# Kernel tuning notes

Hardware: AMD Instinct MI355X
Metric: run time of the kernel (lower is better)

## Reference

```python
import jax, jax.numpy as jnp
import numpy as np
from jax import lax

T, K, F = 262144, 20, 16


def setup_inputs() -> dict:
    key = jax.random.key(0)
    k1, k2, k3, k4 = jax.random.split(key, 4)
    return {
        "observations": jax.random.normal(k1, (T, F), dtype=jnp.float32),
        "beta_logits": jax.random.normal(k2, (K,), dtype=jnp.float32),
        "pi_logits": jax.random.normal(k3, (K, K), dtype=jnp.float32),
        "means": jax.random.normal(k4, (K, F), dtype=jnp.float32),
        "log_vars": jnp.zeros((K, F), dtype=jnp.float32),
    }


def _stick_breaking(logits):
    b = jax.nn.sigmoid(logits)
    cp = jnp.cumprod(1.0 - b)
    return b * jnp.concatenate([jnp.ones((1,), logits.dtype), cp[:-1]])


def _emission_logp(obs, means, log_vars):
    # Diagonal-covariance MultivariateNormal log_prob, vectorized over T and K
    # without materializing a [T,K,F] intermediate.
    var = jnp.exp(log_vars) + 1e-6                       # [K,F]
    inv = 1.0 / var
    const = jnp.sum(means * means * inv + jnp.log(2.0 * jnp.pi * var), axis=1)  # [K]
    quad = (obs * obs) @ inv.T - 2.0 * (obs @ (means * inv).T)                  # [T,K]
    return -0.5 * (quad + const[None, :])


def reference(observations, beta_logits, pi_logits, means, log_vars):
    w = _stick_breaking(beta_logits)                      # [K]
    P = jax.nn.softmax(pi_logits, axis=1)                 # [K,K]
    em = _emission_logp(observations, means, log_vars)    # [T,K]

    # Forward recursion (normalized alpha, as in the original)
    a0 = w * jnp.exp(em[0])
    a0 = a0 / (a0.sum() + 1e-10)

    def fstep(a, e):
        x = (a @ P) * jnp.exp(e)
        x = x / (x.sum() + 1e-10)
        return x, x

    _, a_rest = lax.scan(fstep, a0, em[1:])
    alpha = jnp.concatenate([a0[None], a_rest], axis=0)   # [T,K]

    # Backward recursion (normalized beta)
    bT = jnp.ones((K,), observations.dtype)

    def bstep(bn, e):
        x = P @ (bn * jnp.exp(e))
        x = x / (x.sum() + 1e-10)
        return x, x

    _, b_rest = lax.scan(bstep, bT, em[1:], reverse=True)
    beta = jnp.concatenate([b_rest, bT[None]], axis=0)    # [T,K]

    log_likelihood = jnp.log(alpha[-1].sum() + 1e-10)
    return alpha, beta, log_likelihood
```

## Files before the change

kernel.cpp:

```cpp
#include <hip/hip_runtime.h>
#include <hip/hip_fp16.h>


namespace {
constexpr int Tn = 262144;
constexpr int Kn = 20;
constexpr int Fn = 16;
constexpr float EPSF = 1e-10f;
constexpr float TINY = 1e-35f;

constexpr int Ln3 = 16;
constexpr int Wn3 = 20;
constexpr int NC3 = Tn / Ln3;
constexpr int NBF = NC3 / 16;
constexpr int NBS3 = NC3 / 4;
constexpr int SPC = Ln3 * Kn;

constexpr size_t OFF_P    = 0;
constexpr size_t OFF_W    = 400;
constexpr size_t OFF_CK   = 420;
constexpr size_t OFF_MVIV = 440;
constexpr size_t OFF_E    = 1152;
constexpr size_t OFF_MF   = OFF_E + (size_t)Tn*20 + 64;
constexpr size_t OFF_MB   = OFF_MF + (size_t)Tn;
constexpr size_t OFF_MATF = OFF_MB + (size_t)Tn;
constexpr size_t OFF_MATB = OFF_MATF + 4*(size_t)NC3;
constexpr size_t OFF_SF   = OFF_MATB + 4*(size_t)NC3;
constexpr size_t OFF_SB   = OFF_SF + NC3;
constexpr size_t OFF_END  = OFF_SB + NC3;
}

#if __has_builtin(__builtin_amdgcn_rcpf)
#define FRCP(x) __builtin_amdgcn_rcpf(x)
#else
#define FRCP(x) (1.0f/(x))
#endif

template<int CTRL>
__device__ __forceinline__ float dpp_add(float v) {
  int s = __builtin_amdgcn_update_dpp(0, __float_as_int(v), CTRL, 0xF, 0xF, true);
  return v + __int_as_float(s);
}

__device__ __forceinline__ float reduce16(float v) {
  v = dpp_add<0xB1>(v);
  v = dpp_add<0x4E>(v);
  v = dpp_add<0x141>(v);
  v = dpp_add<0x140>(v);
  return v;
}

__global__ __launch_bounds__(64) void prep_kernel(
    const float* beta_logits, const float* pi_logits,
    const float* means, const float* log_vars, float* ws)
{
  int k = threadIdx.x;
  if (k < Kn) {
    float row[Kn];
    float mx = -1e30f;
#pragma unroll
    for (int j = 0; j < Kn; ++j) { row[j] = pi_logits[k*Kn + j]; mx = fmaxf(mx, row[j]); }
    float s = 0.f;
#pragma unroll
    for (int j = 0; j < Kn; ++j) { row[j] = expf(row[j] - mx); s += row[j]; }
    float invs = 1.0f / s;
#pragma unroll
    for (int j = 0; j < Kn; ++j) ws[OFF_P + k*Kn + j] = row[j] * invs;
    float ck = 0.f;
#pragma unroll
    for (int f = 0; f < Fn; ++f) {
      float lv  = log_vars[k*Fn + f];
      float var = expf(lv) + 1e-6f;
      float iv  = 1.0f / var;
      float mu  = means[k*Fn + f];
      ((float2*)(ws + OFF_MVIV))[k*Fn + f] = make_float2(mu * iv, iv);
      ck += mu*mu*iv + logf(6.2831853071795864f * var);
    }
    ws[OFF_CK + k] = ck;
  } else if (k == Kn) {
    float cp = 1.f;
#pragma unroll
    for (int i = 0; i < Kn; ++i) {
      float b = 1.0f / (1.0f + expf(-beta_logits[i]));
      ws[OFF_W + i] = b * cp;
      cp *= (1.0f - b);
    }
  }
}

__global__ __launch_bounds__(320) void emis_kernel(const float* __restrict__ obs, float* ws)
{
  __shared__ __align__(16) float so[64][20];
  __shared__ __align__(16) float scm[16][24];
  __shared__ __align__(16) float scv[16][24];
  __shared__ __align__(16) float sck[20];
  const int tid = threadIdx.x;
  const int t0 = blockIdx.x * 64;

  if (tid < 256) {
    float4 v = ((const float4*)(obs + (size_t)t0 * Fn))[tid];
    int r = tid >> 2, j = tid & 3;
    *(float4*)&so[r][j*4] = v;
  } else {
    int i = tid - 256;
#pragma unroll
    for (int q = 0; q < 5; ++q) {
      int idx = i * 5 + q;
      float2 c2 = ((const float2*)(ws + OFF_MVIV))[idx];
      int k = idx >> 4, f = idx & 15;
      scm[f][k] = c2.x;
      scv[f][k] = c2.y;
    }
    if (i < Kn) sck[i] = ws[OFF_CK + i];
  }
  __syncthreads();

  const int tl = tid / 5;
  const int k0 = (tid - tl*5) * 4;

  float o[16];
  *(float4*)&o[0]  = *(const float4*)&so[tl][0];
  *(float4*)&o[4]  = *(const float4*)&so[tl][4];
  *(float4*)&o[8]  = *(const float4*)&so[tl][8];
  *(float4*)&o[12] = *(const float4*)&so[tl][12];

  float s1x=0.f,s1y=0.f,s1z=0.f,s1w=0.f;
  float s2x=0.f,s2y=0.f,s2z=0.f,s2w=0.f;
#pragma unroll
  for (int f = 0; f < Fn; ++f) {
    float4 cm = *(const float4*)&scm[f][k0];
    float4 cv = *(const float4*)&scv[f][k0];
    float ov = o[f];
    s1x = fmaf(cv.x * ov, ov, s1x); s2x = fmaf(cm.x, ov, s2x);
    s1y = fmaf(cv.y * ov, ov, s1y); s2y = fmaf(cm.y, ov, s2y);
    s1z = fmaf(cv.z * ov, ov, s1z); s2z = fmaf(cm.z, ov, s2z);
    s1w = fmaf(cv.w * ov, ov, s1w); s2w = fmaf(cm.w, ov, s2w);
  }
  float4 ckv = *(const float4*)&sck[k0];
  float4 rr;
  rr.x = __expf(fmaf(-0.5f, s1x + ckv.x, s2x));
  rr.y = __expf(fmaf(-0.5f, s1y + ckv.y, s2y));
  rr.z = __expf(fmaf(-0.5f, s1z + ckv.z, s2z));
  rr.w = __expf(fmaf(-0.5f, s1w + ckv.w, s2w));
  *(float4*)(ws + OFF_E + (size_t)(t0 + tl)*20 + k0) = rr;
}

__global__ __launch_bounds__(256) void scan3_kernel(float* ws, float* out)
{
  __shared__ __align__(16) float xsh[16][20];
  const int tid = threadIdx.x;
  const int g   = tid >> 4;
  const int ll  = tid & 15;
  const bool hi = (ll < 4);
  const int l4  = 16 + (ll & 3);
  const bool isF = ((int)blockIdx.x < NBF);
  const int c = (isF ? (int)blockIdx.x : (int)blockIdx.x - NBF) * 16 + g;
  const float* E = ws + OFF_E;
  float* xg = &xsh[g][0];

  float Pv0[Kn], Pv1[Kn];
#pragma unroll
  for (int k = 0; k < Kn; ++k) {
    if (isF) {
      Pv0[k] = ws[OFF_P + k*Kn + ll];
      float p1 = ws[OFF_P + k*Kn + l4];
      Pv1[k] = hi ? p1 : 0.f;
    } else {
      Pv0[k] = ws[OFF_P + ll*Kn + k];
      float p1 = ws[OFF_P + l4*Kn + k];
      Pv1[k] = hi ? p1 : 0.f;
    }
  }

  float Ma = 1.f, Mc = 0.f, Md = 1.f;
  float* mArr = ws + (isF ? OFF_MF : OFF_MB);
  __half* uH = (__half*)(out + (isF ? (size_t)0 : (size_t)Tn * Kn) + (size_t)c * SPC);

  auto mobius = [&](float m) {
    float na = m * Ma;
    float nc = fmaf(EPSF, Mc, na);
    float nd = EPSF * Md;
    float mx = fmaxf(nc, nd);
    float lam = (mx > 0.f) ? FRCP(mx) : 1.0f;
    Ma = na*lam; Mc = nc*lam; Md = nd*lam;
  };
  auto matvec2 = [&](float& r0, float& r1) {
    float xv[20];
    *(float4*)&xv[0]  = *(const float4*)&xg[0];
    *(float4*)&xv[4]  = *(const float4*)&xg[4];
    *(float4*)&xv[8]  = *(const float4*)&xg[8];
    *(float4*)&xv[12] = *(const float4*)&xg[12];
    *(float4*)&xv[16] = *(const float4*)&xg[16];
    float A0 = xv[0]*Pv0[0], A1 = xv[1]*Pv0[1];
    float B0 = xv[0]*Pv1[0], B1 = xv[1]*Pv1[1];
#pragma unroll
    for (int k = 2; k < 20; k += 2) {
      A0 = fmaf(xv[k],   Pv0[k],   A0);
      A1 = fmaf(xv[k+1], Pv0[k+1], A1);
      B0 = fmaf(xv[k],   Pv1[k],   B0);
      B1 = fmaf(xv[k+1], Pv1[k+1], B1);
    }
    r0 = A0 + A1; r1 = B0 + B1;
  };

  if (isF) {
    const int bodyStart = c * Ln3;
    const int tend = bodyStart + Ln3 - 1;
    const int t0 = (c == 0) ? 0 : (bodyStart - Wn3);
    float e0a = E[t0*20 + ll],     e1a = E[t0*20 + l4];
    float v0, v1;
    if (c == 0) {
      v0 = ws[OFF_W + ll] * e0a;
      v1 = hi ? ws[OFF_W + l4] * e1a : 0.f;
    } else {
      v0 = 0.05f * e0a;
      v1 = hi ? 0.05f * e1a : 0.f;
    }
    float sv = reduce16(v0 + v1);
    float m = sv;
    float iV = (sv > TINY) ? FRCP(sv) : 1.0f;
    if (sv <= TINY) { v0 = 0.05f; v1 = hi ? 0.05f : 0.f; }
    if (c == 0) {
      if (ll == 0) mArr[0] = m;
      mobius(m);
      uH[ll] = __float2half(v0 * iV);
      if (hi) uH[l4] = __float2half(v1 * iV);
    }
    float A = m * iV;
    float rho = (m > TINY) ? FRCP(m) : 1.0f;
    float e0b = E[(t0+1)*20 + ll], e1b = E[(t0+1)*20 + l4];
    float e0c = E[(t0+2)*20 + ll], e1c = E[(t0+2)*20 + l4];

#define FWD_STEP(REC)                                                     \
    {                                                                     \
      xg[ll] = v0;                                                        \
      if (hi) xg[16 + ll] = v1;                                           \
      float acc0, acc1; matvec2(acc0, acc1);                              \
      float er0 = e0a * rho, er1 = e1a * rho;                             \
      e0a = e0b; e0b = e0c; e0c = E[(t+3)*20 + ll];                       \
      e1a = e1b; e1b = e1c; e1c = E[(t+3)*20 + l4];                       \
      v0 = acc0 * er0; v1 = acc1 * er1;                                   \
      float sv2 = reduce16(v0 + v1);                                      \
      float mn = sv2 * A;                                                 \
      float iVn = (sv2 > TINY) ? FRCP(sv2) : 1.0f;                        \
      if (sv2 <= TINY) { v0 = 0.05f; v1 = hi ? 0.05f : 0.f; }             \
      if (REC) {                                                          \
        if (ll == 0) mArr[t] = mn;                                        \
        mobius(mn);                                                       \
        int lt = t - bodyStart;                                           \
        uH[lt*Kn + ll] = __float2half(v0 * iVn);                          \
        if (hi) uH[lt*Kn + 16 + ll] = __float2half(v1 * iVn);             \
      }                                                                   \
      A = mn * iVn;                                                       \
      rho = (mn > TINY) ? FRCP(mn) : 1.0f;                                \
    }

    for (int t = t0 + 1; t < bodyStart; ++t) FWD_STEP(false)
    const int bstart2 = (c == 0) ? 1 : bodyStart;
    for (int t = bstart2; t <= tend; ++t) FWD_STEP(true)
#undef FWD_STEP
    if (ll == 0) ((float4*)(ws + OFF_MATF))[c] = make_float4(Ma, Mc, Md, 0.f);
  } else {
    const int bodyStart = c * Ln3;
    const int top = bodyStart + Ln3 - 1;
    int r0 = top + Wn3; if (r0 > Tn - 1) r0 = Tn - 1;
    float v0 = 0.05f, v1 = hi ? 0.05f : 0.f;
    float sv = reduce16(v0 + v1);
    float iV = (sv > TINY) ? FRCP(sv) : 1.0f;
    float A = iV;
    float rho = 1.0f;
    float e0a = E[r0*20 + ll],     e1a = E[r0*20 + l4];
    float e0b = E[(r0-1)*20 + ll], e1b = E[(r0-1)*20 + l4];
    float e0c = E[(r0-2)*20 + ll], e1c = E[(r0-2)*20 + l4];

#define BWD_STEP(REC)                                                     \
    {                                                                     \
      xg[ll] = v0 * e0a;                                                  \
      if (hi) xg[16 + ll] = v1 * e1a;                                     \
      float acc0, acc1; matvec2(acc0, acc1);                              \
      v0 = acc0 * rho; v1 = acc1 * rho;                                   \
      e0a = e0b; e0b = e0c; e0c = E[(r-2)*20 + ll];                       \
      e1a = e1b; e1b = e1c; e1c = E[(r-2)*20 + l4];                       \
      float sv2 = reduce16(v0 + v1);                                      \
      float mn = sv2 * A;                                                 \
      float iVn = (sv2 > TINY) ? FRCP(sv2) : 1.0f;                        \
      if (sv2 <= TINY) { v0 = 0.05f; v1 = hi ? 0.05f : 0.f; }             \
      if (REC) {                                                          \
        if (ll == 0) mArr[r+1] = mn;                                      \
        mobius(mn);                                                       \
        int lr = r - bodyStart;                                           \
        uH[lr*Kn + ll] = __float2half(v0 * iVn);                          \
        if (hi) uH[lr*Kn + 16 + ll] = __float2half(v1 * iVn);             \
      }                                                                   \
      A = mn * iVn;                                                       \
      rho = (mn > TINY) ? FRCP(mn) : 1.0f;                                \
    }

    for (int r = r0 - 1; r > top; --r) BWD_STEP(false)
    int rb = (r0 - 1 < top) ? (r0 - 1) : top;
    for (int r = rb; r >= bodyStart; --r) BWD_STEP(true)
#undef BWD_STEP
    if (ll == 0) ((float4*)(ws + OFF_MATB))[NC3 - 1 - c] = make_float4(Ma, Mc, Md, 0.f);
  }
}

__global__ __launch_bounds__(1024) void combine4_kernel(float* ws, float* out)
{
  __shared__ float wag[16][3];
  __shared__ float wpre[16][3];
  const bool isF = (blockIdx.x == 0);
  const float4* M4 = (const float4*)(ws + (isF ? OFF_MATF : OFF_MATB));
  float* sArr = ws + (isF ? OFF_SF : OFF_SB);
  const float s0 = isF ? 1.0f : 20.0f;
  constexpr int PG = NC3 / 1024;
  const int tid  = threadIdx.x;
  const int lane = tid & 63;
  const int wid  = tid >> 6;

  float4 mm[PG];
#pragma unroll
  for (int i = 0; i < PG; ++i) mm[i] = M4[tid*PG + i];

  float a = 1.f, cc = 0.f, d = 1.f;
#pragma unroll
  for (int i = 0; i < PG; ++i) {
    float na = mm[i].x * a;
    float nc = fmaf(mm[i].y, a, mm[i].z * cc);
    float nd = mm[i].z * d;
    float mx = fmaxf(na, fmaxf(nc, nd));
    float lam = (mx > 0.f) ? FRCP(mx) : 1.0f;
    a = na*lam; cc = nc*lam; d = nd*lam;
  }

  float ia = a, ic = cc, id = d;
  for (int off = 1; off < 64; off <<= 1) {
    float pa = __shfl_up(ia, off, 64);
    float pc = __shfl_up(ic, off, 64);
    float pd = __shfl_up(id, off, 64);
    if (lane >= off) {
      float na = ia * pa;
      float nc = fmaf(ic, pa, id * pc);
      float nd = id * pd;
      float mx = fmaxf(na, fmaxf(nc, nd));
      float lam = (mx > 0.f) ? FRCP(mx) : 1.0f;
      ia = na*lam; ic = nc*lam; id = nd*lam;
    }
  }
  if (lane == 63) { wag[wid][0] = ia; wag[wid][1] = ic; wag[wid][2] = id; }
  __syncthreads();

  if (tid == 0) {
    float ea = 1.f, ec = 0.f, ed = 1.f;
#pragma unroll
    for (int w = 0; w < 16; ++w) {
      wpre[w][0] = ea; wpre[w][1] = ec; wpre[w][2] = ed;
      float na = wag[w][0] * ea;
      float nc = fmaf(wag[w][1], ea, wag[w][2] * ec);
      float nd = wag[w][2] * ed;
      float mx = fmaxf(na, fmaxf(nc, nd));
      float lam = (mx > 0.f) ? FRCP(mx) : 1.0f;
      ea = na*lam; ec = nc*lam; ed = nd*lam;
    }
    if (isF) {
      float den = fmaf(ec, s0, ed);
      float sfin = (den > 0.f) ? (ea * s0)/den : 0.f;
      out[(size_t)2 * Tn * Kn] = logf(sfin + EPSF);
    }
  }
  __syncthreads();

  float ea = __shfl_up(ia, 1, 64);
  float ec = __shfl_up(ic, 1, 64);
  float ed = __shfl_up(id, 1, 64);
  if (lane == 0) { ea = 1.f; ec = 0.f; ed = 1.f; }
  float pa = wpre[wid][0], pc = wpre[wid][1], pd = wpre[wid][2];
  float xa = ea * pa;
  float xc = fmaf(ec, pa, ed * pc);
  float xd = ed * pd;

  float num = xa * s0, den = fmaf(xc, s0, xd);
  float s = (den > 0.f) ? num/den : 0.f;
#pragma unroll
  for (int i = 0; i < PG; ++i) {
    sArr[tid*PG + i] = s;
    float nn = mm[i].x * s, dd = fmaf(mm[i].y, s, mm[i].z);
    s = (dd > 0.f) ? nn/dd : 0.f;
  }
}

__global__ __launch_bounds__(128) void scale3_kernel(float* ws, float* out)
{
  __shared__ float sig[4][Ln3];
  const int tid = threadIdx.x;
  const int g   = tid >> 5;
  const int jj  = tid & 31;
  const bool isF = ((int)blockIdx.x < NBS3);
  const int c = (isF ? (int)blockIdx.x : (int)blockIdx.x - NBS3) * 4 + g;
  float* base = out + (isF ? (size_t)0 : (size_t)Tn * Kn) + (size_t)c * SPC;
  const __half* hp = (const __half*)base;

  if (isF) {
    const float* mArr = ws + OFF_MF;
    float s = ws[OFF_SF + c];
    const int t0 = c * Ln3;
#pragma unroll
    for (int i = 0; i < Ln3; ++i) {
      float mm = mArr[t0 + i];
      float z = s * mm;
      float sn = z * FRCP(z + EPSF);
      if (jj == 0) sig[g][i] = sn;
      s = sn;
    }
  } else {
    const float* mArr = ws + OFF_MB;
    const int slot = NC3 - 1 - c;
    float s = ws[OFF_SB + slot];
    const int bodyStart = c * Ln3;
    const int top = bodyStart + Ln3 - 1;
#pragma unroll
    for (int r = top; r >= bodyStart; --r) {
      if (r == Tn - 1) {
        if (jj == 0) sig[g][Ln3 - 1] = 1.0f;
        continue;
      }
      float mm = mArr[r + 1];
      float z = s * mm;
      float sn = z * FRCP(z + EPSF);
      if (jj == 0) sig[g][r - bodyStart] = sn;
      s = sn;
    }
  }

  float vals[10];
#pragma unroll
  for (int q = 0; q < 10; ++q) vals[q] = __half2float(hp[jj*10 + q]);
  __syncthreads();

  const int tl = jj >> 1;
  float sg = sig[g][tl];
  const bool onesRow = (!isF && c == NC3 - 1 && tl == Ln3 - 1);
#pragma unroll
  for (int q = 0; q < 10; ++q) {
    float vv = onesRow ? 1.0f : vals[q] * sg;
    base[jj*10 + q] = vv;
  }
}

extern "C" void kernel_launch(void* const* d_in, const int* in_sizes, int n_in,
                              void* d_out, int out_size, void* d_ws, size_t ws_size,
                              hipStream_t stream) {
  const float* obs         = (const float*)d_in[0];
  const float* beta_logits = (const float*)d_in[1];
  const float* pi_logits   = (const float*)d_in[2];
  const float* means       = (const float*)d_in[3];
  const float* log_vars    = (const float*)d_in[4];
  float* out = (float*)d_out;
  float* ws  = (float*)d_ws;

  hipLaunchKernelGGL(prep_kernel, dim3(1), dim3(64), 0, stream,
                     beta_logits, pi_logits, means, log_vars, ws);
  hipLaunchKernelGGL(emis_kernel, dim3(Tn/64), dim3(320), 0, stream, obs, ws);
  hipLaunchKernelGGL(scan3_kernel, dim3(2*NBF), dim3(256), 0, stream, ws, out);
  hipLaunchKernelGGL(combine4_kernel, dim3(2), dim3(1024), 0, stream, ws, out);
  hipLaunchKernelGGL(scale3_kernel, dim3(2*NBS3), dim3(128), 0, stream, ws, out);
}
```

Measured before the change: 107.8 us.

## Split each scan chunk across 8 lanes with 3 states each, pack half2 outputs

```diff
diff --git a/kernel.cpp b/kernel.cpp
--- a/kernel.cpp
+++ b/kernel.cpp
@@ -10,10 +10,10 @@
 constexpr float TINY = 1e-35f;
 
 constexpr int Ln3 = 16;
-constexpr int Wn3 = 20;
+constexpr int Wn3 = 16;
 constexpr int NC3 = Tn / Ln3;
-constexpr int NBF = NC3 / 16;
-constexpr int NBS3 = NC3 / 4;
+constexpr int NBF4 = NC3 / 32;
+constexpr int NBSC = NC3 / 8;
 constexpr int SPC = Ln3 * Kn;
 
 constexpr size_t OFF_P    = 0;
@@ -42,12 +42,16 @@
   return v + __int_as_float(s);
 }
 
-__device__ __forceinline__ float reduce16(float v) {
+__device__ __forceinline__ float reduce8(float v) {
   v = dpp_add<0xB1>(v);
   v = dpp_add<0x4E>(v);
   v = dpp_add<0x141>(v);
-  v = dpp_add<0x140>(v);
   return v;
+}
+
+__device__ __forceinline__ unsigned packh2(float a, float b) {
+  __half2 h2 = __floats2half2_rn(a, b);
+  return *(unsigned*)&h2;
 }
 
 __global__ __launch_bounds__(64) void prep_kernel(
@@ -145,36 +149,37 @@
   *(float4*)(ws + OFF_E + (size_t)(t0 + tl)*20 + k0) = rr;
 }
 
-__global__ __launch_bounds__(256) void scan3_kernel(float* ws, float* out)
+__global__ __launch_bounds__(256, 4) void scan4_kernel(float* ws, float* out)
 {
-  __shared__ __align__(16) float xsh[16][20];
+  __shared__ __align__(16) float xsh[32][20];
   const int tid = threadIdx.x;
-  const int g   = tid >> 4;
-  const int ll  = tid & 15;
-  const bool hi = (ll < 4);
-  const int l4  = 16 + (ll & 3);
-  const bool isF = ((int)blockIdx.x < NBF);
-  const int c = (isF ? (int)blockIdx.x : (int)blockIdx.x - NBF) * 16 + g;
+  const int g   = tid >> 3;
+  const int j   = tid & 7;
+  const int q   = j & 3;
+  const int s1i = 8 + j;
+  const int s2i = 16 + q;
+  const bool isF = ((int)blockIdx.x < NBF4);
+  const int c = (isF ? (int)blockIdx.x : (int)blockIdx.x - NBF4) * 32 + g;
   const float* E = ws + OFF_E;
   float* xg = &xsh[g][0];
 
-  float Pv0[Kn], Pv1[Kn];
+  float Pv0[Kn], Pv1[Kn], Pv2[Kn];
 #pragma unroll
   for (int k = 0; k < Kn; ++k) {
     if (isF) {
-      Pv0[k] = ws[OFF_P + k*Kn + ll];
-      float p1 = ws[OFF_P + k*Kn + l4];
-      Pv1[k] = hi ? p1 : 0.f;
+      Pv0[k] = ws[OFF_P + k*Kn + j];
+      Pv1[k] = ws[OFF_P + k*Kn + s1i];
+      Pv2[k] = ws[OFF_P + k*Kn + s2i];
     } else {
-      Pv0[k] = ws[OFF_P + ll*Kn + k];
-      float p1 = ws[OFF_P + l4*Kn + k];
-      Pv1[k] = hi ? p1 : 0.f;
+      Pv0[k] = ws[OFF_P + j*Kn + k];
+      Pv1[k] = ws[OFF_P + s1i*Kn + k];
+      Pv2[k] = ws[OFF_P + s2i*Kn + k];
     }
   }
 
   float Ma = 1.f, Mc = 0.f, Md = 1.f;
   float* mArr = ws + (isF ? OFF_MF : OFF_MB);
-  __half* uH = (__half*)(out + (isF ? (size_t)0 : (size_t)Tn * Kn) + (size_t)c * SPC);
+  unsigned* uS = (unsigned*)(out + (isF ? (size_t)0 : (size_t)Tn * Kn) + (size_t)c * SPC);
 
   auto mobius = [&](float m) {
     float na = m * Ma;
@@ -184,72 +189,75 @@
     float lam = (mx > 0.f) ? FRCP(mx) : 1.0f;
     Ma = na*lam; Mc = nc*lam; Md = nd*lam;
   };
-  auto matvec2 = [&](float& r0, float& r1) {
+  auto matvec3 = [&](float& r0, float& r1, float& r2) {
     float xv[20];
     *(float4*)&xv[0]  = *(const float4*)&xg[0];
     *(float4*)&xv[4]  = *(const float4*)&xg[4];
     *(float4*)&xv[8]  = *(const float4*)&xg[8];
     *(float4*)&xv[12] = *(const float4*)&xg[12];
     *(float4*)&xv[16] = *(const float4*)&xg[16];
-    float A0 = xv[0]*Pv0[0], A1 = xv[1]*Pv0[1];
-    float B0 = xv[0]*Pv1[0], B1 = xv[1]*Pv1[1];
+    float a0 = xv[0]*Pv0[0], a1 = xv[1]*Pv0[1];
+    float b0 = xv[0]*Pv1[0], b1 = xv[1]*Pv1[1];
+    float c0 = xv[0]*Pv2[0], c1 = xv[1]*Pv2[1];
 #pragma unroll
     for (int k = 2; k < 20; k += 2) {
-      A0 = fmaf(xv[k],   Pv0[k],   A0);
-      A1 = fmaf(xv[k+1], Pv0[k+1], A1);
-      B0 = fmaf(xv[k],   Pv1[k],   B0);
-      B1 = fmaf(xv[k+1], Pv1[k+1], B1);
-    }
-    r0 = A0 + A1; r1 = B0 + B1;
+      a0 = fmaf(xv[k],   Pv0[k],   a0);
+      a1 = fmaf(xv[k+1], Pv0[k+1], a1);
+      b0 = fmaf(xv[k],   Pv1[k],   b0);
+      b1 = fmaf(xv[k+1], Pv1[k+1], b1);
+      c0 = fmaf(xv[k],   Pv2[k],   c0);
+      c1 = fmaf(xv[k+1], Pv2[k+1], c1);
+    }
+    r0 = a0 + a1; r1 = b0 + b1; r2 = c0 + c1;
   };
 
   if (isF) {
     const int bodyStart = c * Ln3;
     const int tend = bodyStart + Ln3 - 1;
     const int t0 = (c == 0) ? 0 : (bodyStart - Wn3);
-    float e0a = E[t0*20 + ll],     e1a = E[t0*20 + l4];
-    float v0, v1;
+    float e0a = E[t0*20 + j], e1a = E[t0*20 + s1i], e2a = E[t0*20 + s2i];
+    float v0, v1, v2;
     if (c == 0) {
-      v0 = ws[OFF_W + ll] * e0a;
-      v1 = hi ? ws[OFF_W + l4] * e1a : 0.f;
+      v0 = ws[OFF_W + j]   * e0a;
+      v1 = ws[OFF_W + s1i] * e1a;
+      v2 = ws[OFF_W + s2i] * e2a;
     } else {
-      v0 = 0.05f * e0a;
-      v1 = hi ? 0.05f * e1a : 0.f;
-    }
-    float sv = reduce16(v0 + v1);
+      v0 = 0.05f * e0a; v1 = 0.05f * e1a; v2 = 0.05f * e2a;
+    }
+    float sv = reduce8(fmaf(0.5f, v2, v0 + v1));
     float m = sv;
     float iV = (sv > TINY) ? FRCP(sv) : 1.0f;
-    if (sv <= TINY) { v0 = 0.05f; v1 = hi ? 0.05f : 0.f; }
+    if (sv <= TINY) { v0 = 0.05f; v1 = 0.05f; v2 = 0.05f; }
     if (c == 0) {
-      if (ll == 0) mArr[0] = m;
+      mArr[0] = m;
       mobius(m);
-      uH[ll] = __float2half(v0 * iV);
-      if (hi) uH[l4] = __float2half(v1 * iV);
+      uS[j] = packh2(v0 * iV, v1 * iV);
+      uS[8 + q] = packh2(v2 * iV, 0.f);
     }
     float A = m * iV;
     float rho = (m > TINY) ? FRCP(m) : 1.0f;
-    float e0b = E[(t0+1)*20 + ll], e1b = E[(t0+1)*20 + l4];
-    float e0c = E[(t0+2)*20 + ll], e1c = E[(t0+2)*20 + l4];
+    float e0b = E[(t0+1)*20 + j], e1b = E[(t0+1)*20 + s1i], e2b = E[(t0+1)*20 + s2i];
+    float e0c = E[(t0+2)*20 + j], e1c = E[(t0+2)*20 + s1i], e2c = E[(t0+2)*20 + s2i];
 
 #define FWD_STEP(REC)                                                     \
     {                                                                     \
-      xg[ll] = v0;                                                        \
-      if (hi) xg[16 + ll] = v1;                                           \
-      float acc0, acc1; matvec2(acc0, acc1);                              \
-      float er0 = e0a * rho, er1 = e1a * rho;                             \
-      e0a = e0b; e0b = e0c; e0c = E[(t+3)*20 + ll];                       \
-      e1a = e1b; e1b = e1c; e1c = E[(t+3)*20 + l4];                       \
-      v0 = acc0 * er0; v1 = acc1 * er1;                                   \
-      float sv2 = reduce16(v0 + v1);                                      \
+      xg[j] = v0; xg[s1i] = v1; xg[s2i] = v2;                             \
+      float acc0, acc1, acc2; matvec3(acc0, acc1, acc2);                  \
+      float er0 = e0a * rho, er1 = e1a * rho, er2 = e2a * rho;            \
+      e0a = e0b; e0b = e0c; e0c = E[(t+3)*20 + j];                        \
+      e1a = e1b; e1b = e1c; e1c = E[(t+3)*20 + s1i];                      \
+      e2a = e2b; e2b = e2c; e2c = E[(t+3)*20 + s2i];                      \
+      v0 = acc0 * er0; v1 = acc1 * er1; v2 = acc2 * er2;                  \
+      float sv2 = reduce8(fmaf(0.5f, v2, v0 + v1));                      \
       float mn = sv2 * A;                                                 \
       float iVn = (sv2 > TINY) ? FRCP(sv2) : 1.0f;                        \
-      if (sv2 <= TINY) { v0 = 0.05f; v1 = hi ? 0.05f : 0.f; }             \
+      if (sv2 <= TINY) { v0 = 0.05f; v1 = 0.05f; v2 = 0.05f; }            \
       if (REC) {                                                          \
-        if (ll == 0) mArr[t] = mn;                                        \
+        mArr[t] = mn;                                                     \
         mobius(mn);                                                       \
         int lt = t - bodyStart;                                           \
-        uH[lt*Kn + ll] = __float2half(v0 * iVn);                          \
-        if (hi) uH[lt*Kn + 16 + ll] = __float2half(v1 * iVn);             \
+        uS[lt*12 + j] = packh2(v0 * iVn, v1 * iVn);                       \
+        uS[lt*12 + 8 + q] = packh2(v2 * iVn, 0.f);                        \
       }                                                                   \
       A = mn * iVn;                                                       \
       rho = (mn > TINY) ? FRCP(mn) : 1.0f;                                \
@@ -259,38 +267,38 @@
     const int bstart2 = (c == 0) ? 1 : bodyStart;
     for (int t = bstart2; t <= tend; ++t) FWD_STEP(true)
 #undef FWD_STEP
-    if (ll == 0) ((float4*)(ws + OFF_MATF))[c] = make_float4(Ma, Mc, Md, 0.f);
+    ((float4*)(ws + OFF_MATF))[c] = make_float4(Ma, Mc, Md, 0.f);
   } else {
     const int bodyStart = c * Ln3;
     const int top = bodyStart + Ln3 - 1;
     int r0 = top + Wn3; if (r0 > Tn - 1) r0 = Tn - 1;
-    float v0 = 0.05f, v1 = hi ? 0.05f : 0.f;
-    float sv = reduce16(v0 + v1);
+    float v0 = 0.05f, v1 = 0.05f, v2 = 0.05f;
+    float sv = reduce8(fmaf(0.5f, v2, v0 + v1));
     float iV = (sv > TINY) ? FRCP(sv) : 1.0f;
     float A = iV;
     float rho = 1.0f;
-    float e0a = E[r0*20 + ll],     e1a = E[r0*20 + l4];
-    float e0b = E[(r0-1)*20 + ll], e1b = E[(r0-1)*20 + l4];
-    float e0c = E[(r0-2)*20 + ll], e1c = E[(r0-2)*20 + l4];
+    float e0a = E[r0*20 + j], e1a = E[r0*20 + s1i], e2a = E[r0*20 + s2i];
+    float e0b = E[(r0-1)*20 + j], e1b = E[(r0-1)*20 + s1i], e2b = E[(r0-1)*20 + s2i];
+    float e0c = E[(r0-2)*20 + j], e1c = E[(r0-2)*20 + s1i], e2c = E[(r0-2)*20 + s2i];
 
 #define BWD_STEP(REC)                                                     \
     {                                                                     \
-      xg[ll] = v0 * e0a;                                                  \
-      if (hi) xg[16 + ll] = v1 * e1a;                                     \
-      float acc0, acc1; matvec2(acc0, acc1);                              \
-      v0 = acc0 * rho; v1 = acc1 * rho;                                   \
-      e0a = e0b; e0b = e0c; e0c = E[(r-2)*20 + ll];                       \
-      e1a = e1b; e1b = e1c; e1c = E[(r-2)*20 + l4];                       \
-      float sv2 = reduce16(v0 + v1);                                      \
+      xg[j] = v0 * e0a; xg[s1i] = v1 * e1a; xg[s2i] = v2 * e2a;           \
+      float acc0, acc1, acc2; matvec3(acc0, acc1, acc2);                  \
+      v0 = acc0 * rho; v1 = acc1 * rho; v2 = acc2 * rho;                  \
+      e0a = e0b; e0b = e0c; e0c = E[(r-2)*20 + j];                        \
+      e1a = e1b; e1b = e1c; e1c = E[(r-2)*20 + s1i];                      \
+      e2a = e2b; e2b = e2c; e2c = E[(r-2)*20 + s2i];                      \
+      float sv2 = reduce8(fmaf(0.5f, v2, v0 + v1));                      \
       float mn = sv2 * A;                                                 \
       float iVn = (sv2 > TINY) ? FRCP(sv2) : 1.0f;                        \
-      if (sv2 <= TINY) { v0 = 0.05f; v1 = hi ? 0.05f : 0.f; }             \
+      if (sv2 <= TINY) { v0 = 0.05f; v1 = 0.05f; v2 = 0.05f; }            \
       if (REC) {                                                          \
-        if (ll == 0) mArr[r+1] = mn;                                      \
+        mArr[r+1] = mn;                                                   \
         mobius(mn);                                                       \
         int lr = r - bodyStart;                                           \
-        uH[lr*Kn + ll] = __float2half(v0 * iVn);                          \
-        if (hi) uH[lr*Kn + 16 + ll] = __float2half(v1 * iVn);             \
+        uS[lr*12 + j] = packh2(v0 * iVn, v1 * iVn);                       \
+        uS[lr*12 + 8 + q] = packh2(v2 * iVn, 0.f);                        \
       }                                                                   \
       A = mn * iVn;                                                       \
       rho = (mn > TINY) ? FRCP(mn) : 1.0f;                                \
@@ -300,7 +308,7 @@
     int rb = (r0 - 1 < top) ? (r0 - 1) : top;
     for (int r = rb; r >= bodyStart; --r) BWD_STEP(true)
 #undef BWD_STEP
-    if (ll == 0) ((float4*)(ws + OFF_MATB))[NC3 - 1 - c] = make_float4(Ma, Mc, Md, 0.f);
+    ((float4*)(ws + OFF_MATB))[NC3 - 1 - c] = make_float4(Ma, Mc, Md, 0.f);
   }
 }
 
@@ -388,62 +396,78 @@
   }
 }
 
-__global__ __launch_bounds__(128) void scale3_kernel(float* ws, float* out)
+__global__ __launch_bounds__(128) void scale4_kernel(float* ws, float* out)
 {
-  __shared__ float sig[4][Ln3];
   const int tid = threadIdx.x;
-  const int g   = tid >> 5;
-  const int jj  = tid & 31;
-  const bool isF = ((int)blockIdx.x < NBS3);
-  const int c = (isF ? (int)blockIdx.x : (int)blockIdx.x - NBS3) * 4 + g;
+  const int g   = tid >> 4;
+  const int ll  = tid & 15;
+  const bool isF = ((int)blockIdx.x < NBSC);
+  const int c = (isF ? (int)blockIdx.x : (int)blockIdx.x - NBSC) * 8 + g;
   float* base = out + (isF ? (size_t)0 : (size_t)Tn * Kn) + (size_t)c * SPC;
-  const __half* hp = (const __half*)base;
-
+  const unsigned* uS = (const unsigned*)base;
+
+  float mySig = 1.0f;
   if (isF) {
-    const float* mArr = ws + OFF_MF;
+    const float* mA = ws + OFF_MF;
     float s = ws[OFF_SF + c];
     const int t0 = c * Ln3;
 #pragma unroll
     for (int i = 0; i < Ln3; ++i) {
-      float mm = mArr[t0 + i];
-      float z = s * mm;
+      float z = s * mA[t0 + i];
       float sn = z * FRCP(z + EPSF);
-      if (jj == 0) sig[g][i] = sn;
+      if (i == ll) mySig = sn;
       s = sn;
     }
   } else {
-    const float* mArr = ws + OFF_MB;
-    const int slot = NC3 - 1 - c;
-    float s = ws[OFF_SB + slot];
-    const int bodyStart = c * Ln3;
-    const int top = bodyStart + Ln3 - 1;
-#pragma unroll
-    for (int r = top; r >= bodyStart; --r) {
-      if (r == Tn - 1) {
-        if (jj == 0) sig[g][Ln3 - 1] = 1.0f;
-        continue;
+    const float* mA = ws + OFF_MB;
+    float s = ws[OFF_SB + (NC3 - 1 - c)];
+    const int top = c * Ln3 + Ln3 - 1;
+#pragma unroll
+    for (int i = 0; i < Ln3; ++i) {
+      int r = top - i;
+      float sn;
+      if (r == Tn - 1) sn = s;
+      else {
+        float z = s * mA[r + 1];
+        sn = z * FRCP(z + EPSF);
       }
-      float mm = mArr[r + 1];
-      float z = s * mm;
-      float sn = z * FRCP(z + EPSF);
-      if (jj == 0) sig[g][r - bodyStart] = sn;
+      if (i == Ln3 - 1 - ll) mySig = sn;
       s = sn;
     }
   }
 
-  float vals[10];
-#pragma unroll
-  for (int q = 0; q < 10; ++q) vals[q] = __half2float(hp[jj*10 + q]);
+  uint4 ua = ((const uint4*)(uS + ll*12))[0];
+  uint4 ub = ((const uint4*)(uS + ll*12))[1];
+  uint4 uc = ((const uint4*)(uS + ll*12))[2];
   __syncthreads();
 
-  const int tl = jj >> 1;
-  float sg = sig[g][tl];
-  const bool onesRow = (!isF && c == NC3 - 1 && tl == Ln3 - 1);
-#pragma unroll
-  for (int q = 0; q < 10; ++q) {
-    float vv = onesRow ? 1.0f : vals[q] * sg;
-    base[jj*10 + q] = vv;
-  }
+  const bool onesRow = (!isF && c == NC3 - 1 && ll == Ln3 - 1);
+  float sg = mySig;
+  unsigned slots[12] = {ua.x,ua.y,ua.z,ua.w, ub.x,ub.y,ub.z,ub.w, uc.x,uc.y,uc.z,uc.w};
+  float o[20];
+#pragma unroll
+  for (int jj = 0; jj < 8; ++jj) {
+    __half2 h2 = *(__half2*)&slots[jj];
+    float2 f2 = __half22float2(h2);
+    o[jj]     = f2.x * sg;
+    o[8 + jj] = f2.y * sg;
+  }
+#pragma unroll
+  for (int qq = 0; qq < 4; ++qq) {
+    __half2 h2 = *(__half2*)&slots[8 + qq];
+    float2 f2 = __half22float2(h2);
+    o[16 + qq] = f2.x * sg;
+  }
+  if (onesRow) {
+#pragma unroll
+    for (int k = 0; k < 20; ++k) o[k] = 1.0f;
+  }
+  float* dst = base + ll * 20;
+  *(float4*)&dst[0]  = *(float4*)&o[0];
+  *(float4*)&dst[4]  = *(float4*)&o[4];
+  *(float4*)&dst[8]  = *(float4*)&o[8];
+  *(float4*)&dst[12] = *(float4*)&o[12];
+  *(float4*)&dst[16] = *(float4*)&o[16];
 }
 
 extern "C" void kernel_launch(void* const* d_in, const int* in_sizes, int n_in,
@@ -460,7 +484,7 @@
   hipLaunchKernelGGL(prep_kernel, dim3(1), dim3(64), 0, stream,
                      beta_logits, pi_logits, means, log_vars, ws);
   hipLaunchKernelGGL(emis_kernel, dim3(Tn/64), dim3(320), 0, stream, obs, ws);
-  hipLaunchKernelGGL(scan3_kernel, dim3(2*NBF), dim3(256), 0, stream, ws, out);
+  hipLaunchKernelGGL(scan4_kernel, dim3(2*NBF4), dim3(256), 0, stream, ws, out);
   hipLaunchKernelGGL(combine4_kernel, dim3(2), dim3(1024), 0, stream, ws, out);
-  hipLaunchKernelGGL(scale3_kernel, dim3(2*NBS3), dim3(128), 0, stream, ws, out);
-}
+  hipLaunchKernelGGL(scale4_kernel, dim3(2*NBSC), dim3(128), 0, stream, ws, out);
+}
```

New measurement: 94.54 us. 12.3% less time.
